# Optimization experiments

Hardware: AMD Instinct MI355X
Metric: run time of the kernel (lower is better)

## Reference

```python
import jax, jax.numpy as jnp
import numpy as np

B, N, D = 32, 2048, 320

def _init(key, shape, fan_in):
    return jax.random.normal(key, shape, dtype=jnp.float32) / np.sqrt(fan_in).astype(np.float32)

def setup_inputs() -> dict:
    key = jax.random.key(0)
    ks = jax.random.split(key, 11)
    return {
        "x": jax.random.normal(ks[0], (B, N, D), dtype=jnp.float32),
        # downs MLP: 320->160->80
        "W1": _init(ks[1], (320, 160), 320), "b1": jnp.zeros((160,), jnp.float32),
        "W2": _init(ks[2], (160, 80), 160),  "b2": jnp.zeros((80,), jnp.float32),
        # GraphConv1d layers: 80->40, 40->5
        "Wg1": _init(ks[3], (80, 40), 80),   "bg1": jnp.zeros((40,), jnp.float32),
        "Wg2": _init(ks[4], (40, 5), 40),    "bg2": jnp.zeros((5,), jnp.float32),
        # final classifier: 5->2
        "Wf": _init(ks[5], (5, 2), 5),       "bf": jnp.zeros((2,), jnp.float32),
    }

def _euclidean_adj(h):
    # h: [B, N, C] -> row-softmax of negative squared pairwise Euclidean distance [B, N, N]
    sq = jnp.sum(h * h, axis=-1, keepdims=True)               # [B, N, 1]
    d2 = sq - 2.0 * jnp.einsum('bnc,bmc->bnm', h, h) + jnp.swapaxes(sq, -1, -2)
    return jax.nn.softmax(-d2, axis=-1)

def _graph_conv(h, W, b):
    a = _euclidean_adj(h)                                     # dynamic adjacency
    agg = jnp.einsum('bnm,bmc->bnc', a, h)                    # neighbor aggregation
    return jax.nn.relu(agg @ W + b)

def reference(x, W1, b1, W2, b2, Wg1, bg1, Wg2, bg2, Wf, bf):
    h = jax.nn.relu(x @ W1 + b1)          # [B, N, 160]
    h = jax.nn.relu(h @ W2 + b2)          # [B, N, 80]
    h = _graph_conv(h, Wg1, bg1)          # [B, N, 40]
    h = _graph_conv(h, Wg2, bg2)          # [B, N, 5]
    h = jnp.mean(h, axis=1)               # Mean() over nodes -> [B, 5]
    logits = h @ Wf + bf                  # [B, 2]
    return jax.nn.softmax(logits, axis=-1)
```

## Files before the change

kernel.cpp:

```cpp
#include <hip/hip_runtime.h>
#include <math.h>

#define BB 32
#define NN 2048
#define D_IN 320
#define H1 160
#define H2 80
#define H4 5

typedef __attribute__((ext_vector_type(8))) short short8;
typedef __attribute__((ext_vector_type(4))) short short4v;
typedef __attribute__((ext_vector_type(4))) float f32x4;
typedef __attribute__((ext_vector_type(16))) float f32x16;

__device__ inline ushort f2bf(float f) {
    union { float f; unsigned u; } v; v.f = f;
    unsigned r = v.u + 0x7fff + ((v.u >> 16) & 1);
    return (ushort)(r >> 16);
}
__device__ inline float bf2f(ushort u) {
    union { float f; unsigned u; } v; v.u = ((unsigned)u) << 16;
    return v.f;
}
__device__ inline unsigned pkbf(float hi, float lo) {
    union { float f; unsigned u; } a, b; a.f = hi; b.f = lo;
    return __builtin_amdgcn_perm(a.u + 0x8000u, b.u + 0x8000u, 0x07060302u);
}
__device__ inline float fexp2(float x) {
    float r;
    asm("v_exp_f32 %0, %1" : "=v"(r) : "v"(x));
    return r;
}
union U2S { unsigned u[2]; short4v s; };
union U4S { unsigned u[4]; short8 s; short4v h[2]; };

#define LOG2E  1.44269504088896340736f
#define TWOL2E 2.88539008177792681472f

__global__ __launch_bounds__(256) void prep_weights_kernel(
    const float* __restrict__ W1, const float* __restrict__ W2,
    const float* __restrict__ Wg1, const float* __restrict__ bg1,
    const float* __restrict__ Wg2, const float* __restrict__ bg2,
    ushort* __restrict__ Wt1, ushort* __restrict__ Wt2,
    ushort* __restrict__ Wg1T, float* __restrict__ bg1P,
    ushort* __restrict__ Wg2T, float* __restrict__ bg2P)
{
    const int id0 = blockIdx.x * 256 + threadIdx.x;
    const int stride = gridDim.x * 256;
    for (int i = id0; i < H1 * D_IN; i += stride) {
        const int j = i / D_IN, c = i % D_IN;
        Wt1[i] = f2bf(W1[c * H1 + j]);
    }
    for (int i = id0; i < H2 * H1; i += stride) {
        const int j = i / H1, c = i % H1;
        Wt2[i] = f2bf(W2[c * H2 + j]);
    }
    for (int i = id0; i < 64 * 96; i += stride) {
        const int j = i / 96, c = i % 96;
        const int c4 = c & 15;
        const int pos = (c & ~15) + (c4 & 3) + (((c4 >> 3) & 1) << 2) + (((c4 >> 2) & 1) << 3);
        Wg1T[j * 96 + pos] = (j < 40 && c < 80) ? f2bf(Wg1[c * 40 + j]) : (ushort)0;
    }
    for (int i = id0; i < 32 * 64; i += stride) {
        const int j = i / 64, c = i % 64;
        const int c4 = c & 15;
        const int pos = (c & ~15) + (c4 & 3) + (((c4 >> 3) & 1) << 2) + (((c4 >> 2) & 1) << 3);
        Wg2T[j * 64 + pos] = (j < 5 && c < 40) ? f2bf(Wg2[c * 5 + j]) : (ushort)0;
    }
    if (id0 < 64) bg1P[id0] = (id0 < 40) ? bg1[id0] : 0.f;
    if (id0 < 32) bg2P[id0] = (id0 < 5) ? bg2[id0] : 0.f;
}

__global__ __launch_bounds__(256) void mlp_mfma_kernel(
    const float* __restrict__ x,
    const ushort* __restrict__ Wt1, const float* __restrict__ b1,
    const ushort* __restrict__ Wt2, const float* __restrict__ b2,
    ushort* __restrict__ h2, ushort* __restrict__ h2T, float* __restrict__ sq2)
{
    constexpr int XST  = 72;
    constexpr int W1ST = 72;
    constexpr int H1ST = 168;

    __shared__ __attribute__((aligned(16))) ushort h1t[64 * H1ST];
    __shared__ __attribute__((aligned(16))) ushort ws1[H1 * W1ST];
    __shared__ float b1s[H1];
    __shared__ float b2s[H2];

    ushort* xs = h1t;

    const int t = threadIdx.x;
    const int lane = t & 63, w = t >> 6;
    const int colid = lane & 15, quad = lane >> 4;
    const int i = blockIdx.x;
    const int b = ((i & 7) << 2) + ((i >> 3) & 3);
    const int n0 = (i >> 5) * 64;
    const int row0 = b * NN + n0;

    if (t < H1) b1s[t] = b1[t];
    if (t < H2) b2s[t] = b2[t];

    f32x4 c1[10];
    #pragma unroll
    for (int ns = 0; ns < 10; ++ns) c1[ns] = (f32x4){0.f, 0.f, 0.f, 0.f};

    float4 xr[4];
    short8 wr[5];
    {
        #pragma unroll
        for (int i2 = 0; i2 < 4; ++i2) {
            const int id = t + i2 * 256, row = id >> 4, c4 = id & 15;
            xr[i2] = *(const float4*)&x[(size_t)(row0 + row) * D_IN + c4 * 4];
        }
        #pragma unroll
        for (int i2 = 0; i2 < 5; ++i2) {
            const int id = t + i2 * 256, j = id >> 3, part = id & 7;
            wr[i2] = *(const short8*)&Wt1[j * D_IN + part * 8];
        }
    }

    for (int kc = 0; kc < 5; ++kc) {
        if (kc) __syncthreads();
        #pragma unroll
        for (int i2 = 0; i2 < 4; ++i2) {
            const int id = t + i2 * 256, row = id >> 4, c4 = id & 15;
            uint2 up;
            up.x = pkbf(xr[i2].y, xr[i2].x);
            up.y = pkbf(xr[i2].w, xr[i2].z);
            *(uint2*)&xs[row * XST + c4 * 4] = up;
        }
        #pragma unroll
        for (int i2 = 0; i2 < 5; ++i2) {
            const int id = t + i2 * 256, j = id >> 3, part = id & 7;
            *(short8*)&ws1[j * W1ST + part * 8] = wr[i2];
        }
        __syncthreads();
        if (kc < 4) {
            const int k0 = (kc + 1) * 64;
            #pragma unroll
            for (int i2 = 0; i2 < 4; ++i2) {
                const int id = t + i2 * 256, row = id >> 4, c4 = id & 15;
                xr[i2] = *(const float4*)&x[(size_t)(row0 + row) * D_IN + k0 + c4 * 4];
            }
            #pragma unroll
            for (int i2 = 0; i2 < 5; ++i2) {
                const int id = t + i2 * 256, j = id >> 3, part = id & 7;
                wr[i2] = *(const short8*)&Wt1[j * D_IN + k0 + part * 8];
            }
        }

        short8 af[2];
        #pragma unroll
        for (int kf = 0; kf < 2; ++kf)
            af[kf] = *(const short8*)&xs[(w * 16 + colid) * XST + kf * 32 + quad * 8];
        #pragma unroll
        for (int ns = 0; ns < 10; ++ns) {
            #pragma unroll
            for (int kf = 0; kf < 2; ++kf) {
                const short8 bf = *(const short8*)&ws1[(ns * 16 + colid) * W1ST + kf * 32 + quad * 8];
                c1[ns] = __builtin_amdgcn_mfma_f32_16x16x32_bf16(af[kf], bf, c1[ns], 0, 0, 0);
            }
        }
    }
    __syncthreads();

    #pragma unroll
    for (int ns = 0; ns < 10; ++ns) {
        const float bj = b1s[ns * 16 + colid];
        #pragma unroll
        for (int r = 0; r < 4; ++r)
            h1t[(w * 16 + quad * 4 + r) * H1ST + ns * 16 + colid] =
                f2bf(fmaxf(c1[ns][r] + bj, 0.f));
    }
    __asm__ volatile("s_waitcnt lgkmcnt(0)" ::: "memory");

    short8 a2[5];
    #pragma unroll
    for (int kf = 0; kf < 5; ++kf)
        a2[kf] = *(const short8*)&h1t[(w * 16 + colid) * H1ST + kf * 32 + quad * 8];

    f32x4 c2[5];
    #pragma unroll
    for (int js = 0; js < 5; ++js) {
        f32x4 acc = (f32x4){0.f, 0.f, 0.f, 0.f};
        #pragma unroll
        for (int kf = 0; kf < 5; ++kf) {
            const short8 wb = *(const short8*)&Wt2[(js * 16 + colid) * H1 + kf * 32 + quad * 8];
            acc = __builtin_amdgcn_mfma_f32_16x16x32_bf16(a2[kf], wb, acc, 0, 0, 0);
        }
        c2[js] = acc;
    }
    __syncthreads();

    ushort* Tbuf = ws1;
    float rsq[4] = {0.f, 0.f, 0.f, 0.f};
    #pragma unroll
    for (int js = 0; js < 5; ++js) {
        const float bj = b2s[js * 16 + colid];
        #pragma unroll
        for (int r = 0; r < 4; ++r) {
            const ushort u = f2bf(fmaxf(c2[js][r] + bj, 0.f));
            const float vv = bf2f(u);
            rsq[r] += vv * vv;
            h2[(size_t)(row0 + w * 16 + quad * 4 + r) * 80 + js * 16 + colid] = u;
            Tbuf[(js * 16 + colid) * 72 + w * 16 + quad * 4 + r] = u;
        }
    }
    {
        const short8 z8 = {0, 0, 0, 0, 0, 0, 0, 0};
        const short8 ones8 = {16256, 16256, 16256, 16256, 16256, 16256, 16256, 16256};
        if (t < 128) {
            const int row = 80 + (t >> 3), part = t & 7;
            *(short8*)&Tbuf[row * 72 + part * 8] = (row == 80) ? ones8 : z8;
        }
    }
    #pragma unroll
    for (int m = 1; m <= 8; m <<= 1)
        #pragma unroll
        for (int r = 0; r < 4; ++r) rsq[r] += __shfl_xor(rsq[r], m);
    if (colid == 0) {
        #pragma unroll
        for (int r = 0; r < 4; ++r)
            sq2[(size_t)row0 + w * 16 + quad * 4 + r] = rsq[r] * LOG2E;
    }
    __syncthreads();
    for (int id = t; id < 96 * 8; id += 256) {
        const int row = id >> 3, part = id & 7;
        *(short8*)&h2T[((size_t)b * 96 + row) * NN + n0 + part * 8] =
            *(const short8*)&Tbuf[row * 72 + part * 8];
    }
}

template<int CK, int CV, int C_OUT, int JT, int ONES_CH, bool HAS_OUT, bool DO_MEAN>
__global__ __launch_bounds__(256, 2) void attn_conv_kernel(
    const ushort* __restrict__ h, const ushort* __restrict__ hT,
    const float* __restrict__ sqg,
    const ushort* __restrict__ WtG, const float* __restrict__ biasP,
    ushort* __restrict__ ho, ushort* __restrict__ hoT, float* __restrict__ sqo,
    float* __restrict__ mean_out)
{
    constexpr int CFP  = CV / 16;
    constexpr int CF   = CK / 16;
    constexpr int CSV  = CV / 32;
    constexpr int KST  = CK + 8;
    constexpr int VST  = 64 + 8;
    constexpr int KPR  = CK / 8;
    constexpr int KTOT = 64 * KPR;
    constexpr int NK   = (KTOT + 255) / 256;
    constexpr int NV   = (CV * 8) / 256;
    constexpr int TST  = 136;
    constexpr int CS1  = ONES_CH / 32;
    constexpr int R1   = ((ONES_CH % 32) / 8) * 4 + (ONES_CH & 3);
    constexpr int BUFN = 64 * KST + CV * VST;

    __shared__ __attribute__((aligned(16))) ushort ldsbuf[2][BUFN];
    __shared__ __attribute__((aligned(16))) float sqs[2][64];

    const int t = threadIdx.x;
    const int lane = t & 63, w = t >> 6;
    const int m32 = lane & 31, hl = lane >> 5;
    const int i = blockIdx.x;
    const int b = ((i & 7) << 2) + ((i >> 3) & 3);
    const int n0blk = (i >> 5) * 128;
    const int qrow = n0blk + w * 32 + m32;

    short8 qf[CF];
    {
        const ushort* qr = h + ((size_t)b * NN + qrow) * CK;
        #pragma unroll
        for (int c = 0; c < CF; ++c)
            qf[c] = *(const short8*)&qr[c * 16 + hl * 8];
    }
    const float nsqnQL = -sqg[(size_t)b * NN + qrow];

    f32x16 o[CSV];
    #pragma unroll
    for (int cs = 0; cs < CSV; ++cs)
        #pragma unroll
        for (int r = 0; r < 16; ++r) o[cs][r] = 0.f;

    short8 kreg[NK], vreg[NV];
    float sqreg = 0.f;

    auto loadTile = [&](int n1) {
        const ushort* hsrc = h + ((size_t)b * NN + n1) * CK;
        #pragma unroll
        for (int i2 = 0; i2 < NK; ++i2) {
            const int id = t + i2 * 256;
            if (KTOT % 256 == 0 || id < KTOT)
                kreg[i2] = *(const short8*)&hsrc[id * 8];
        }
        #pragma unroll
        for (int i2 = 0; i2 < NV; ++i2) {
            const int id = t + i2 * 256, c = id >> 3, pt = id & 7;
            vreg[i2] = *(const short8*)&hT[((size_t)b * CV + c) * NN + n1 + pt * 8];
        }
        if (t < 64) sqreg = sqg[(size_t)b * NN + n1 + t];
    };
    auto stageTile = [&](int buf) {
        ushort* Kd = ldsbuf[buf];
        ushort* Vd = ldsbuf[buf] + 64 * KST;
        #pragma unroll
        for (int i2 = 0; i2 < NK; ++i2) {
            const int id = t + i2 * 256;
            if (KTOT % 256 == 0 || id < KTOT) {
                const int row = id / KPR, pt = id % KPR;
                *(short8*)&Kd[row * KST + pt * 8] = kreg[i2];
            }
        }
        #pragma unroll
        for (int i2 = 0; i2 < NV; ++i2) {
            const int id = t + i2 * 256, c = id >> 3, pt = id & 7;
            const int colb = ((pt >> 1) << 4) + ((pt & 1) << 2);
            U4S vv; vv.s = vreg[i2];
            *(short4v*)&Vd[c * VST + colb]     = vv.h[0];
            *(short4v*)&Vd[c * VST + colb + 8] = vv.h[1];
        }
        if (t < 64) sqs[buf][t] = sqreg;
    };

    loadTile(0);
    stageTile(0);
    __syncthreads();
    loadTile(64);

    for (int it = 0; it < NN / 64; ++it) {
        const int cur = it & 1;
        const ushort* Krow = ldsbuf[cur];
        const ushort* Vcol = ldsbuf[cur] + 64 * KST;

        short8 kf_[2][CF];
        short8 vf_[2][2][CSV];
        f32x4  smv_[2][4];
        #pragma unroll
        for (int T = 0; T < 2; ++T) {
            #pragma unroll
            for (int c = 0; c < CF; ++c)
                kf_[T][c] = *(const short8*)&Krow[(T * 32 + m32) * KST + c * 16 + hl * 8];
            #pragma unroll
            for (int c = 0; c < 2; ++c)
                #pragma unroll
                for (int cs = 0; cs < CSV; ++cs)
                    vf_[T][c][cs] = *(const short8*)&Vcol[(cs * 32 + m32) * VST + (T * 2 + c) * 16 + hl * 8];
            #pragma unroll
            for (int g = 0; g < 4; ++g)
                smv_[T][g] = *(const f32x4*)&sqs[cur][T * 32 + g * 8 + hl * 4];
        }

        if (it + 1 < NN / 64) {
            stageTile(cur ^ 1);
            if (it + 2 < NN / 64) loadTile((it + 2) * 64);
        }

        f32x16 st0, st1;
        #pragma unroll
        for (int r = 0; r < 16; ++r) { st0[r] = 0.f; st1[r] = 0.f; }
        #pragma unroll
        for (int c = 0; c < CF; ++c) {
            st0 = __builtin_amdgcn_mfma_f32_32x32x16_bf16(kf_[0][c], qf[c], st0, 0, 0, 0);
            st1 = __builtin_amdgcn_mfma_f32_32x32x16_bf16(kf_[1][c], qf[c], st1, 0, 0, 0);
        }

        #pragma unroll
        for (int T = 0; T < 2; ++T) {
            const f32x16& st = T ? st1 : st0;
            float p[16];
            #pragma unroll
            for (int g = 0; g < 4; ++g) {
                #pragma unroll
                for (int r2 = 0; r2 < 4; ++r2)
                    p[g * 4 + r2] = fexp2(fmaf(st[g * 4 + r2], TWOL2E,
                                               nsqnQL - smv_[T][g][r2]));
            }
            #pragma unroll
            for (int c = 0; c < 2; ++c) {
                U4S pk_;
                #pragma unroll
                for (int bq = 0; bq < 4; ++bq)
                    pk_.u[bq] = pkbf(p[c * 8 + bq * 2 + 1], p[c * 8 + bq * 2]);
                #pragma unroll
                for (int cs = 0; cs < CSV; ++cs)
                    o[cs] = __builtin_amdgcn_mfma_f32_32x32x16_bf16(vf_[T][c][cs], pk_.s, o[cs], 0, 0, 0);
            }
        }
        __syncthreads();
    }

    float rsv = (hl == 0) ? o[CS1][R1] : 0.f;
    rsv += __shfl_xor(rsv, 32);
    const float rinv = 1.f / rsv;

    short8 ob[CFP];
    #pragma unroll
    for (int cs = 0; cs < CSV; ++cs)
        #pragma unroll
        for (int c2 = 0; c2 < 2; ++c2) {
            U4S ob_;
            #pragma unroll
            for (int bq = 0; bq < 4; ++bq)
                ob_.u[bq] = pkbf(o[cs][c2 * 8 + bq * 2 + 1] * rinv,
                                 o[cs][c2 * 8 + bq * 2] * rinv);
            ob[cs * 2 + c2] = ob_.s;
        }

    ushort* Tbuf = (ushort*)ldsbuf;
    float rsq = 0.f;
    float msum[4] = {0.f, 0.f, 0.f, 0.f};

    #pragma unroll
    for (int jt = 0; jt < JT; ++jt) {
        f32x16 acc;
        #pragma unroll
        for (int r = 0; r < 16; ++r) acc[r] = 0.f;
        #pragma unroll
        for (int cc = 0; cc < CFP; ++cc) {
            const short8 wa = *(const short8*)&WtG[(size_t)(jt * 32 + m32) * CV + cc * 16 + hl * 8];
            acc = __builtin_amdgcn_mfma_f32_32x32x16_bf16(wa, ob[cc], acc, 0, 0, 0);
        }
        #pragma unroll
        for (int g = 0; g < 4; ++g) {
            const f32x4 bv = *(const f32x4*)&biasP[jt * 32 + g * 8 + hl * 4];
            float v[4];
            #pragma unroll
            for (int r2 = 0; r2 < 4; ++r2) {
                v[r2] = fmaxf(acc[g * 4 + r2] + bv[r2], 0.f);
                rsq += v[r2] * v[r2];
            }
            if (HAS_OUT) {
                U2S uo;
                uo.u[0] = pkbf(v[1], v[0]);
                uo.u[1] = pkbf(v[3], v[2]);
                const int jb = jt * 32 + g * 8 + hl * 4;
                if (jb < 48)
                    *(short4v*)&ho[((size_t)b * NN + qrow) * 48 + jb] = uo.s;
                const int qc = w * 32 + m32;
                #pragma unroll
                for (int r2 = 0; r2 < 4; ++r2)
                    Tbuf[(jb + r2) * TST + qc] =
                        (ushort)(uo.u[r2 >> 1] >> ((r2 & 1) * 16));
            }
            if (DO_MEAN && jt == 0 && g == 0) {
                #pragma unroll
                for (int r2 = 0; r2 < 4; ++r2) msum[r2] = v[r2];
            }
        }
    }

    if (HAS_OUT) {
        const float rsq2 = rsq + __shfl_xor(rsq, 32);
        if (hl == 0) sqo[(size_t)b * NN + qrow] = rsq2 * LOG2E;
        __syncthreads();
        const short8 ones8 = {16256, 16256, 16256, 16256, 16256, 16256, 16256, 16256};
        for (int id = t; id < 64 * 16; id += 256) {
            const int row = id >> 4, part = id & 15;
            const short8 val = (row == 40) ? ones8
                             : *(const short8*)&Tbuf[row * TST + part * 8];
            *(short8*)&hoT[((size_t)b * 64 + row) * NN + n0blk + part * 8] = val;
        }
    }
    if (DO_MEAN) {
        #pragma unroll
        for (int s = 1; s <= 16; s <<= 1)
            #pragma unroll
            for (int r2 = 0; r2 < 4; ++r2) msum[r2] += __shfl_xor(msum[r2], s);
        if (m32 == 0) {
            if (hl == 0) {
                #pragma unroll
                for (int r2 = 0; r2 < 4; ++r2)
                    atomicAdd(&mean_out[b * C_OUT + r2], msum[r2] * (1.f / NN));
            } else {
                atomicAdd(&mean_out[b * C_OUT + 4], msum[0] * (1.f / NN));
            }
        }
    }
}

__global__ __launch_bounds__(64) void final_kernel(
    const float* __restrict__ mean, const float* __restrict__ Wf,
    const float* __restrict__ bf, float* __restrict__ out)
{
    const int t = threadIdx.x;
    const int b = t >> 1, k = t & 1;
    float acc = bf[k];
    #pragma unroll
    for (int c = 0; c < H4; ++c) acc += mean[b * H4 + c] * Wf[c * 2 + k];
    const float other = __shfl_xor(acc, 1);
    const float mx = fmaxf(acc, other);
    const float e  = __expf(acc - mx);
    const float eo = __expf(other - mx);
    out[t] = e / (e + eo);
}

extern "C" void kernel_launch(void* const* d_in, const int* in_sizes, int n_in,
                              void* d_out, int out_size, void* d_ws, size_t ws_size,
                              hipStream_t stream) {
    const float* x   = (const float*)d_in[0];
    const float* W1  = (const float*)d_in[1];
    const float* b1  = (const float*)d_in[2];
    const float* W2  = (const float*)d_in[3];
    const float* b2  = (const float*)d_in[4];
    const float* Wg1 = (const float*)d_in[5];
    const float* bg1 = (const float*)d_in[6];
    const float* Wg2 = (const float*)d_in[7];
    const float* bg2 = (const float*)d_in[8];
    const float* Wf  = (const float*)d_in[9];
    const float* bf  = (const float*)d_in[10];

    ushort* h2   = (ushort*)d_ws;
    ushort* h2T  = h2  + (size_t)BB * NN * 80;
    float*  sq2  = (float*)(h2T + (size_t)BB * 96 * NN);
    ushort* h3   = (ushort*)(sq2 + (size_t)BB * NN);
    ushort* h3T  = h3  + (size_t)BB * NN * 48;
    float*  sq3  = (float*)(h3T + (size_t)BB * 64 * NN);
    float*  meanb = sq3 + (size_t)BB * NN;
    ushort* Wt1  = (ushort*)(meanb + 160);
    ushort* Wt2  = Wt1 + (size_t)H1 * D_IN;
    ushort* Wg1T = Wt2 + (size_t)H2 * H1;
    float*  bg1P = (float*)(Wg1T + 64 * 96);
    ushort* Wg2T = (ushort*)(bg1P + 64);
    float*  bg2P = (float*)(Wg2T + 32 * 64);

    hipMemsetAsync(meanb, 0, BB * H4 * sizeof(float), stream);

    prep_weights_kernel<<<64, 256, 0, stream>>>(W1, W2, Wg1, bg1, Wg2, bg2,
                                                Wt1, Wt2, Wg1T, bg1P, Wg2T, bg2P);
    mlp_mfma_kernel<<<BB * NN / 64, 256, 0, stream>>>(x, Wt1, b1, Wt2, b2, h2, h2T, sq2);
    attn_conv_kernel<80, 96, 40, 2, 80, true,  false><<<BB * NN / 128, 256, 0, stream>>>(
        h2, h2T, sq2, Wg1T, bg1P, h3, h3T, sq3, nullptr);
    attn_conv_kernel<48, 64, 5, 1, 40, false, true><<<BB * NN / 128, 256, 0, stream>>>(
        h3, h3T, sq3, Wg2T, bg2P, nullptr, nullptr, nullptr, meanb);
    final_kernel<<<1, 64, 0, stream>>>(meanb, Wf, bf, (float*)d_out);
}
```

Baseline: 269.1 us.

## Apply graph-conv weights before aggregation to shrink value channels

Uses associativity (A·h)·W = A·(h·W): the projection by Wg1 moves into the MLP kernel, and the projection by Wg2 moves into the first attention kernel's epilogue. The value tensors the attention kernels aggregate therefore shrink from 96 to 48 and from 64 to 16 channels. This cuts MFMA work in the attention-times-V products and the bytes of transposed value data written and read, and it leaves each attention kernel with only a bias plus ReLU on the aggregated output. In exchange the projected values are rounded to bf16 before aggregation rather than after, and the kernels gain extra MFMA and LDS passes.

```diff
diff --git a/kernel.cpp b/kernel.cpp
--- a/kernel.cpp
+++ b/kernel.cpp
@@ -42,8 +42,8 @@
     const float* __restrict__ Wg1, const float* __restrict__ bg1,
     const float* __restrict__ Wg2, const float* __restrict__ bg2,
     ushort* __restrict__ Wt1, ushort* __restrict__ Wt2,
-    ushort* __restrict__ Wg1T, float* __restrict__ bg1P,
-    ushort* __restrict__ Wg2T, float* __restrict__ bg2P)
+    ushort* __restrict__ Wg1B, float* __restrict__ bg1P,
+    ushort* __restrict__ Wg2A, float* __restrict__ bg2P)
 {
     const int id0 = blockIdx.x * 256 + threadIdx.x;
     const int stride = gridDim.x * 256;
@@ -55,17 +55,15 @@
         const int j = i / H1, c = i % H1;
         Wt2[i] = f2bf(W2[c * H2 + j]);
     }
-    for (int i = id0; i < 64 * 96; i += stride) {
+    for (int i = id0; i < 48 * 96; i += stride) {
         const int j = i / 96, c = i % 96;
+        Wg1B[i] = (j < 40 && c < 80) ? f2bf(Wg1[c * 40 + j]) : (ushort)0;
+    }
+    for (int i = id0; i < 32 * 48; i += stride) {
+        const int j = i / 48, c = i % 48;
         const int c4 = c & 15;
         const int pos = (c & ~15) + (c4 & 3) + (((c4 >> 3) & 1) << 2) + (((c4 >> 2) & 1) << 3);
-        Wg1T[j * 96 + pos] = (j < 40 && c < 80) ? f2bf(Wg1[c * 40 + j]) : (ushort)0;
-    }
-    for (int i = id0; i < 32 * 64; i += stride) {
-        const int j = i / 64, c = i % 64;
-        const int c4 = c & 15;
-        const int pos = (c & ~15) + (c4 & 3) + (((c4 >> 3) & 1) << 2) + (((c4 >> 2) & 1) << 3);
-        Wg2T[j * 64 + pos] = (j < 5 && c < 40) ? f2bf(Wg2[c * 5 + j]) : (ushort)0;
+        Wg2A[j * 48 + pos] = (j < 5 && c < 40) ? f2bf(Wg2[c * 5 + j]) : (ushort)0;
     }
     if (id0 < 64) bg1P[id0] = (id0 < 40) ? bg1[id0] : 0.f;
     if (id0 < 32) bg2P[id0] = (id0 < 5) ? bg2[id0] : 0.f;
@@ -75,11 +73,13 @@
     const float* __restrict__ x,
     const ushort* __restrict__ Wt1, const float* __restrict__ b1,
     const ushort* __restrict__ Wt2, const float* __restrict__ b2,
-    ushort* __restrict__ h2, ushort* __restrict__ h2T, float* __restrict__ sq2)
+    const ushort* __restrict__ Wg1B,
+    ushort* __restrict__ h2, ushort* __restrict__ V1T, float* __restrict__ sq2)
 {
     constexpr int XST  = 72;
     constexpr int W1ST = 72;
     constexpr int H1ST = 168;
+    constexpr int RST  = 104;
 
     __shared__ __attribute__((aligned(16))) ushort h1t[64 * H1ST];
     __shared__ __attribute__((aligned(16))) ushort ws1[H1 * W1ST];
@@ -191,7 +191,7 @@
     }
     __syncthreads();
 
-    ushort* Tbuf = ws1;
+    ushort* h2row = h1t;
     float rsq[4] = {0.f, 0.f, 0.f, 0.f};
     #pragma unroll
     for (int js = 0; js < 5; ++js) {
@@ -202,17 +202,32 @@
             const float vv = bf2f(u);
             rsq[r] += vv * vv;
             h2[(size_t)(row0 + w * 16 + quad * 4 + r) * 80 + js * 16 + colid] = u;
-            Tbuf[(js * 16 + colid) * 72 + w * 16 + quad * 4 + r] = u;
+            h2row[(w * 16 + quad * 4 + r) * RST + js * 16 + colid] = u;
         }
     }
     {
-        const short8 z8 = {0, 0, 0, 0, 0, 0, 0, 0};
-        const short8 ones8 = {16256, 16256, 16256, 16256, 16256, 16256, 16256, 16256};
-        if (t < 128) {
-            const int row = 80 + (t >> 3), part = t & 7;
-            *(short8*)&Tbuf[row * 72 + part * 8] = (row == 80) ? ones8 : z8;
-        }
-    }
+        const int zr = t >> 2, zc = t & 3;
+        *(short4v*)&h2row[zr * RST + 80 + zc * 4] = (short4v){0, 0, 0, 0};
+    }
+    __asm__ volatile("s_waitcnt lgkmcnt(0)" ::: "memory");
+
+    short8 a3[3];
+    #pragma unroll
+    for (int kf = 0; kf < 3; ++kf)
+        a3[kf] = *(const short8*)&h2row[(w * 16 + colid) * RST + kf * 32 + quad * 8];
+
+    f32x4 c3[3];
+    #pragma unroll
+    for (int js = 0; js < 3; ++js) {
+        f32x4 acc = (f32x4){0.f, 0.f, 0.f, 0.f};
+        #pragma unroll
+        for (int kf = 0; kf < 3; ++kf) {
+            const short8 wb = *(const short8*)&Wg1B[(js * 16 + colid) * 96 + kf * 32 + quad * 8];
+            acc = __builtin_amdgcn_mfma_f32_16x16x32_bf16(a3[kf], wb, acc, 0, 0, 0);
+        }
+        c3[js] = acc;
+    }
+
     #pragma unroll
     for (int m = 1; m <= 8; m <<= 1)
         #pragma unroll
@@ -222,23 +237,30 @@
         for (int r = 0; r < 4; ++r)
             sq2[(size_t)row0 + w * 16 + quad * 4 + r] = rsq[r] * LOG2E;
     }
+
+    ushort* Tbuf = ws1;
+    #pragma unroll
+    for (int js = 0; js < 3; ++js)
+        #pragma unroll
+        for (int r = 0; r < 4; ++r)
+            Tbuf[(js * 16 + colid) * 72 + w * 16 + quad * 4 + r] = f2bf(c3[js][r]);
     __syncthreads();
-    for (int id = t; id < 96 * 8; id += 256) {
+    const short8 ones8 = {16256, 16256, 16256, 16256, 16256, 16256, 16256, 16256};
+    for (int id = t; id < 48 * 8; id += 256) {
         const int row = id >> 3, part = id & 7;
-        *(short8*)&h2T[((size_t)b * 96 + row) * NN + n0 + part * 8] =
-            *(const short8*)&Tbuf[row * 72 + part * 8];
-    }
-}
-
-template<int CK, int CV, int C_OUT, int JT, int ONES_CH, bool HAS_OUT, bool DO_MEAN>
+        const short8 val = (row == 40) ? ones8 : *(const short8*)&Tbuf[row * 72 + part * 8];
+        *(short8*)&V1T[((size_t)b * 48 + row) * NN + n0 + part * 8] = val;
+    }
+}
+
+template<int CK, int CV, int CVS, int ONES_CH, bool HAS_OUT, bool DO_MEAN, int C_OUT>
 __global__ __launch_bounds__(256, 2) void attn_conv_kernel(
     const ushort* __restrict__ h, const ushort* __restrict__ hT,
     const float* __restrict__ sqg,
-    const ushort* __restrict__ WtG, const float* __restrict__ biasP,
+    const ushort* __restrict__ WtP, const float* __restrict__ biasP,
     ushort* __restrict__ ho, ushort* __restrict__ hoT, float* __restrict__ sqo,
     float* __restrict__ mean_out)
 {
-    constexpr int CFP  = CV / 16;
     constexpr int CF   = CK / 16;
     constexpr int CSV  = CV / 32;
     constexpr int KST  = CK + 8;
@@ -292,7 +314,9 @@
         #pragma unroll
         for (int i2 = 0; i2 < NV; ++i2) {
             const int id = t + i2 * 256, c = id >> 3, pt = id & 7;
-            vreg[i2] = *(const short8*)&hT[((size_t)b * CV + c) * NN + n1 + pt * 8];
+            vreg[i2] = (c < CVS)
+                ? *(const short8*)&hT[((size_t)b * CVS + c) * NN + n1 + pt * 8]
+                : (short8){0, 0, 0, 0, 0, 0, 0, 0};
         }
         if (t < 64) sqreg = sqg[(size_t)b * NN + n1 + t];
     };
@@ -389,75 +413,11 @@
     rsv += __shfl_xor(rsv, 32);
     const float rinv = 1.f / rsv;
 
-    short8 ob[CFP];
-    #pragma unroll
-    for (int cs = 0; cs < CSV; ++cs)
-        #pragma unroll
-        for (int c2 = 0; c2 < 2; ++c2) {
-            U4S ob_;
-            #pragma unroll
-            for (int bq = 0; bq < 4; ++bq)
-                ob_.u[bq] = pkbf(o[cs][c2 * 8 + bq * 2 + 1] * rinv,
-                                 o[cs][c2 * 8 + bq * 2] * rinv);
-            ob[cs * 2 + c2] = ob_.s;
-        }
-
-    ushort* Tbuf = (ushort*)ldsbuf;
-    float rsq = 0.f;
-    float msum[4] = {0.f, 0.f, 0.f, 0.f};
-
-    #pragma unroll
-    for (int jt = 0; jt < JT; ++jt) {
-        f32x16 acc;
-        #pragma unroll
-        for (int r = 0; r < 16; ++r) acc[r] = 0.f;
-        #pragma unroll
-        for (int cc = 0; cc < CFP; ++cc) {
-            const short8 wa = *(const short8*)&WtG[(size_t)(jt * 32 + m32) * CV + cc * 16 + hl * 8];
-            acc = __builtin_amdgcn_mfma_f32_32x32x16_bf16(wa, ob[cc], acc, 0, 0, 0);
-        }
-        #pragma unroll
-        for (int g = 0; g < 4; ++g) {
-            const f32x4 bv = *(const f32x4*)&biasP[jt * 32 + g * 8 + hl * 4];
-            float v[4];
-            #pragma unroll
-            for (int r2 = 0; r2 < 4; ++r2) {
-                v[r2] = fmaxf(acc[g * 4 + r2] + bv[r2], 0.f);
-                rsq += v[r2] * v[r2];
-            }
-            if (HAS_OUT) {
-                U2S uo;
-                uo.u[0] = pkbf(v[1], v[0]);
-                uo.u[1] = pkbf(v[3], v[2]);
-                const int jb = jt * 32 + g * 8 + hl * 4;
-                if (jb < 48)
-                    *(short4v*)&ho[((size_t)b * NN + qrow) * 48 + jb] = uo.s;
-                const int qc = w * 32 + m32;
-                #pragma unroll
-                for (int r2 = 0; r2 < 4; ++r2)
-                    Tbuf[(jb + r2) * TST + qc] =
-                        (ushort)(uo.u[r2 >> 1] >> ((r2 & 1) * 16));
-            }
-            if (DO_MEAN && jt == 0 && g == 0) {
-                #pragma unroll
-                for (int r2 = 0; r2 < 4; ++r2) msum[r2] = v[r2];
-            }
-        }
-    }
-
-    if (HAS_OUT) {
-        const float rsq2 = rsq + __shfl_xor(rsq, 32);
-        if (hl == 0) sqo[(size_t)b * NN + qrow] = rsq2 * LOG2E;
-        __syncthreads();
-        const short8 ones8 = {16256, 16256, 16256, 16256, 16256, 16256, 16256, 16256};
-        for (int id = t; id < 64 * 16; id += 256) {
-            const int row = id >> 4, part = id & 15;
-            const short8 val = (row == 40) ? ones8
-                             : *(const short8*)&Tbuf[row * TST + part * 8];
-            *(short8*)&hoT[((size_t)b * 64 + row) * NN + n0blk + part * 8] = val;
-        }
-    }
-    if (DO_MEAN) {
+    if constexpr (DO_MEAN) {
+        float msum[4];
+        #pragma unroll
+        for (int r2 = 0; r2 < 4; ++r2)
+            msum[r2] = fmaxf(o[0][r2] * rinv + biasP[hl * 4 + r2], 0.f);
         #pragma unroll
         for (int s = 1; s <= 16; s <<= 1)
             #pragma unroll
@@ -470,6 +430,70 @@
             } else {
                 atomicAdd(&mean_out[b * C_OUT + 4], msum[0] * (1.f / NN));
             }
+        }
+    }
+
+    if constexpr (HAS_OUT) {
+        float vv[CSV][16];
+        float rsq = 0.f;
+        #pragma unroll
+        for (int cs = 0; cs < CSV; ++cs) {
+            #pragma unroll
+            for (int g = 0; g < 4; ++g) {
+                const int jb = cs * 32 + g * 8 + hl * 4;
+                const f32x4 bv = *(const f32x4*)&biasP[jb];
+                float v[4];
+                #pragma unroll
+                for (int r2 = 0; r2 < 4; ++r2) {
+                    float val = fmaxf(o[cs][g * 4 + r2] * rinv + bv[r2], 0.f);
+                    if (cs == CS1 && g * 4 + r2 == R1) val = 0.f;
+                    v[r2] = val;
+                    rsq += val * val;
+                    vv[cs][g * 4 + r2] = val;
+                }
+                if (jb < 48) {
+                    U2S uo;
+                    uo.u[0] = pkbf(v[1], v[0]);
+                    uo.u[1] = pkbf(v[3], v[2]);
+                    *(short4v*)&ho[((size_t)b * NN + qrow) * 48 + jb] = uo.s;
+                }
+            }
+        }
+        const float rsq2 = rsq + __shfl_xor(rsq, 32);
+        if (hl == 0) sqo[(size_t)b * NN + qrow] = rsq2 * LOG2E;
+
+        short8 ob2[3];
+        #pragma unroll
+        for (int cc = 0; cc < 3; ++cc) {
+            const int cs = cc >> 1, c2 = cc & 1;
+            U4S ob_;
+            #pragma unroll
+            for (int bq = 0; bq < 4; ++bq)
+                ob_.u[bq] = pkbf(vv[cs][c2 * 8 + bq * 2 + 1], vv[cs][c2 * 8 + bq * 2]);
+            ob2[cc] = ob_.s;
+        }
+        f32x16 acc;
+        #pragma unroll
+        for (int r = 0; r < 16; ++r) acc[r] = 0.f;
+        #pragma unroll
+        for (int cc = 0; cc < 3; ++cc) {
+            const short8 wa = *(const short8*)&WtP[(size_t)m32 * 48 + cc * 16 + hl * 8];
+            acc = __builtin_amdgcn_mfma_f32_32x32x16_bf16(wa, ob2[cc], acc, 0, 0, 0);
+        }
+
+        ushort* Tbuf = (ushort*)ldsbuf;
+        #pragma unroll
+        for (int g = 0; g < 2; ++g)
+            #pragma unroll
+            for (int r2 = 0; r2 < 4; ++r2)
+                Tbuf[(g * 8 + hl * 4 + r2) * TST + w * 32 + m32] = f2bf(acc[g * 4 + r2]);
+        __syncthreads();
+        const short8 ones8 = {16256, 16256, 16256, 16256, 16256, 16256, 16256, 16256};
+        {
+            const int row = t >> 4, part = t & 15;
+            const short8 val = (row == 8) ? ones8
+                             : *(const short8*)&Tbuf[row * TST + part * 8];
+            *(short8*)&hoT[((size_t)b * 16 + row) * NN + n0blk + part * 8] = val;
         }
     }
 }
@@ -506,27 +530,28 @@
     const float* bf  = (const float*)d_in[10];
 
     ushort* h2   = (ushort*)d_ws;
-    ushort* h2T  = h2  + (size_t)BB * NN * 80;
-    float*  sq2  = (float*)(h2T + (size_t)BB * 96 * NN);
+    ushort* V1T  = h2  + (size_t)BB * NN * 80;
+    float*  sq2  = (float*)(V1T + (size_t)BB * 48 * NN);
     ushort* h3   = (ushort*)(sq2 + (size_t)BB * NN);
-    ushort* h3T  = h3  + (size_t)BB * NN * 48;
-    float*  sq3  = (float*)(h3T + (size_t)BB * 64 * NN);
+    ushort* V2T  = h3  + (size_t)BB * NN * 48;
+    float*  sq3  = (float*)(V2T + (size_t)BB * 16 * NN);
     float*  meanb = sq3 + (size_t)BB * NN;
     ushort* Wt1  = (ushort*)(meanb + 160);
     ushort* Wt2  = Wt1 + (size_t)H1 * D_IN;
-    ushort* Wg1T = Wt2 + (size_t)H2 * H1;
-    float*  bg1P = (float*)(Wg1T + 64 * 96);
-    ushort* Wg2T = (ushort*)(bg1P + 64);
-    float*  bg2P = (float*)(Wg2T + 32 * 64);
+    ushort* Wg1B = Wt2 + (size_t)H2 * H1;
+    float*  bg1P = (float*)(Wg1B + 48 * 96);
+    ushort* Wg2A = (ushort*)(bg1P + 64);
+    float*  bg2P = (float*)(Wg2A + 32 * 48);
 
     hipMemsetAsync(meanb, 0, BB * H4 * sizeof(float), stream);
 
     prep_weights_kernel<<<64, 256, 0, stream>>>(W1, W2, Wg1, bg1, Wg2, bg2,
-                                                Wt1, Wt2, Wg1T, bg1P, Wg2T, bg2P);
-    mlp_mfma_kernel<<<BB * NN / 64, 256, 0, stream>>>(x, Wt1, b1, Wt2, b2, h2, h2T, sq2);
-    attn_conv_kernel<80, 96, 40, 2, 80, true,  false><<<BB * NN / 128, 256, 0, stream>>>(
-        h2, h2T, sq2, Wg1T, bg1P, h3, h3T, sq3, nullptr);
-    attn_conv_kernel<48, 64, 5, 1, 40, false, true><<<BB * NN / 128, 256, 0, stream>>>(
-        h3, h3T, sq3, Wg2T, bg2P, nullptr, nullptr, nullptr, meanb);
+                                                Wt1, Wt2, Wg1B, bg1P, Wg2A, bg2P);
+    mlp_mfma_kernel<<<BB * NN / 64, 256, 0, stream>>>(x, Wt1, b1, Wt2, b2, Wg1B,
+                                                      h2, V1T, sq2);
+    attn_conv_kernel<80, 64, 48, 40, true,  false, 0><<<BB * NN / 128, 256, 0, stream>>>(
+        h2, V1T, sq2, Wg2A, bg1P, h3, V2T, sq3, nullptr);
+    attn_conv_kernel<48, 32, 16, 8,  false, true,  5><<<BB * NN / 128, 256, 0, stream>>>(
+        h3, V2T, sq3, nullptr, bg2P, nullptr, nullptr, nullptr, meanb);
     final_kernel<<<1, 64, 0, stream>>>(meanb, Wf, bf, (float*)d_out);
 }
```

New measurement: 258.4 us. 4.0% less time.
